# Kernel optimization log

Hardware: AMD Instinct MI355X
Metric: run time of the kernel (lower is better)

Reference implementation:

```python
import jax, jax.numpy as jnp
import numpy as np

S, B, C, H = 2048, 2, 512, 8
CC = C // H


def setup_inputs() -> dict:
    key = jax.random.key(0)
    ks = jax.random.split(key, 8)
    x = jax.random.normal(ks[0], (S, B, C), dtype=jnp.float32)
    pe = jax.random.normal(ks[1], (S, B, C), dtype=jnp.float32)
    # strict causal mask: True means masked-out (future positions t > s)
    idx = jnp.arange(S)
    content_mask = (idx[None, :] > idx[:, None])  # (s, t)
    content_mask = jnp.broadcast_to(content_mask[:, :, None], (S, S, B))
    pad = jnp.full((B,), S, dtype=jnp.int64)  # full-length sequences (unused in training path)
    scale = 0.02
    Wqkv = jax.random.normal(ks[2], (3 * C, C), dtype=jnp.float32) * scale
    bqkv = jax.random.normal(ks[3], (3 * C,), dtype=jnp.float32) * scale
    Wc = jax.random.normal(ks[4], (C, C), dtype=jnp.float32) * scale
    bc = jax.random.normal(ks[5], (C,), dtype=jnp.float32) * scale
    return {"x": x, "pe": pe, "content_mask": content_mask, "pad": pad,
            "Wqkv": Wqkv, "bqkv": bqkv, "Wc": Wc, "bc": bc}


def reference(x, pe, content_mask, pad, Wqkv, bqkv, Wc, bc):
    s, b, c = x.shape
    h, cc = H, CC
    qkv = jnp.einsum('sbc,dc->sbd', x + pe, Wqkv) + bqkv  # (s, b, 3c)
    q, k, v = jnp.split(qkv, 3, axis=-1)
    q = q.reshape(s, b, h, cc)
    k = k.reshape(s, b, h, cc)
    v = v.reshape(s, b, h, cc)
    temperature = 1.0 / np.sqrt(cc).astype(np.float32)
    qk = jnp.einsum('sbhc,tbhc->stbh', q, k) * temperature  # (s, t, b, h)
    a = jnp.where(content_mask[:, :, :, None], -jnp.inf, qk)
    p = jax.nn.softmax(a, axis=1)  # softmax over t (dim=1), matching torch
    out = jnp.einsum('stbh,tbhc->sbhc', p, v).reshape(s, b, c)
    out = jnp.einsum('sbc,dc->sbd', out, Wc) + bc
    return out
```

## Files before the change

kernel.cpp:

```cpp
#include <hip/hip_runtime.h>
#include <hip/hip_bf16.h>

#define S_LEN 2048
#define BATCH 2
#define CDIM  512
#define HEADS 8
#define HDIM  64
#define QKVD  1536

typedef float          f32x4  __attribute__((ext_vector_type(4)));
typedef __bf16         bf16x8 __attribute__((ext_vector_type(8)));
typedef unsigned short u16x8  __attribute__((ext_vector_type(8)));

typedef __attribute__((address_space(1))) const unsigned int* gas_ptr;
typedef __attribute__((address_space(3))) unsigned int* las_ptr;

static __device__ __forceinline__ unsigned short f2bf(float x) {
  union { float f; unsigned u; } v; v.f = x;
  unsigned r = v.u + 0x7fffu + ((v.u >> 16) & 1u);
  return (unsigned short)(r >> 16);
}
static __device__ __forceinline__ float bf2f(unsigned short x) {
  union { unsigned u; float f; } v; v.u = (unsigned)x << 16;
  return v.f;
}

__global__ void __launch_bounds__(256) prep_kernel(
    const float* __restrict__ x, const float* __restrict__ pe,
    const float* __restrict__ wqkv, const float* __restrict__ wc,
    unsigned short* __restrict__ xpe_bf,
    unsigned short* __restrict__ wqkv_bf,
    unsigned short* __restrict__ wc_bf) {
  const int N1 = S_LEN * BATCH * CDIM;
  const int N2 = QKVD * CDIM;
  const int NP = (N1 + N2 + CDIM * CDIM) / 8;
  const int pkt = blockIdx.x * 256 + threadIdx.x;
  if (pkt >= NP) return;
  int i = pkt * 8;
  u16x8 o;
  if (i < N1) {
    f32x4 a0 = *reinterpret_cast<const f32x4*>(x + i);
    f32x4 a1 = *reinterpret_cast<const f32x4*>(x + i + 4);
    f32x4 b0 = *reinterpret_cast<const f32x4*>(pe + i);
    f32x4 b1 = *reinterpret_cast<const f32x4*>(pe + i + 4);
#pragma unroll
    for (int j = 0; j < 4; ++j) { o[j] = f2bf(a0[j] + b0[j]); o[4 + j] = f2bf(a1[j] + b1[j]); }
    *reinterpret_cast<u16x8*>(xpe_bf + i) = o;
  } else if (i < N1 + N2) {
    i -= N1;
    f32x4 a0 = *reinterpret_cast<const f32x4*>(wqkv + i);
    f32x4 a1 = *reinterpret_cast<const f32x4*>(wqkv + i + 4);
#pragma unroll
    for (int j = 0; j < 4; ++j) { o[j] = f2bf(a0[j]); o[4 + j] = f2bf(a1[j]); }
    *reinterpret_cast<u16x8*>(wqkv_bf + i) = o;
  } else {
    i -= N1 + N2;
    f32x4 a0 = *reinterpret_cast<const f32x4*>(wc + i);
    f32x4 a1 = *reinterpret_cast<const f32x4*>(wc + i + 4);
#pragma unroll
    for (int j = 0; j < 4; ++j) { o[j] = f2bf(a0[j]); o[4 + j] = f2bf(a1[j]); }
    *reinterpret_cast<u16x8*>(wc_bf + i) = o;
  }
}

template <int BM, int BN, int OUT_BF16>
__global__ void __launch_bounds__(256) gemm_lds_kernel(
    const unsigned short* __restrict__ A,
    const unsigned short* __restrict__ Bt,
    const float* __restrict__ bias,
    void* __restrict__ Cout, int M, int N, int K) {
  constexpr int FM = BM / 32;
  constexpr int FN = BN / 32;
  __shared__ unsigned short Alds[BM * 64];
  __shared__ unsigned short Blds[BN * 64];

  const int tid  = threadIdx.x;
  const int w    = tid >> 6;
  const int lane = tid & 63;
  const int wr   = w >> 1, wc = w & 1;
  const int lr   = lane & 15, hi = lane >> 4;
  const int m0   = blockIdx.y * BM;
  const int n0   = blockIdx.x * BN;

  f32x4 acc[FM][FN];
#pragma unroll
  for (int fm = 0; fm < FM; ++fm)
#pragma unroll
    for (int fn = 0; fn < FN; ++fn) acc[fm][fn] = (f32x4){0.f, 0.f, 0.f, 0.f};

  for (int kc = 0; kc < K; kc += 64) {
    __syncthreads();
#pragma unroll
    for (int i = 0; i < BM / 32; ++i) {
      const int idx = tid + i * 256;
      const int row = idx >> 3, col = (idx & 7) * 8;
      const int scol = col ^ ((row & 7) * 8);
      __builtin_amdgcn_global_load_lds(
          (gas_ptr)(const void*)(A + (size_t)(m0 + row) * K + kc + scol),
          (las_ptr)(void*)(Alds + idx * 8), 16, 0, 0);
    }
#pragma unroll
    for (int i = 0; i < BN / 32; ++i) {
      const int idx = tid + i * 256;
      const int row = idx >> 3, col = (idx & 7) * 8;
      const int scol = col ^ ((row & 7) * 8);
      __builtin_amdgcn_global_load_lds(
          (gas_ptr)(const void*)(Bt + (size_t)(n0 + row) * K + kc + scol),
          (las_ptr)(void*)(Blds + idx * 8), 16, 0, 0);
    }
    __syncthreads();

    bf16x8 af[2][FM], bfr[2][FN];
#pragma unroll
    for (int ks = 0; ks < 2; ++ks) {
#pragma unroll
      for (int fm = 0; fm < FM; ++fm) {
        const int row = wr * (BM / 2) + fm * 16 + lr;
        af[ks][fm] = *reinterpret_cast<const bf16x8*>(
            &Alds[row * 64 + ((ks * 32 + hi * 8) ^ ((row & 7) * 8))]);
      }
#pragma unroll
      for (int fn = 0; fn < FN; ++fn) {
        const int row = wc * (BN / 2) + fn * 16 + lr;
        bfr[ks][fn] = *reinterpret_cast<const bf16x8*>(
            &Blds[row * 64 + ((ks * 32 + hi * 8) ^ ((row & 7) * 8))]);
      }
    }
#pragma unroll
    for (int ks = 0; ks < 2; ++ks)
#pragma unroll
      for (int fm = 0; fm < FM; ++fm)
#pragma unroll
        for (int fn = 0; fn < FN; ++fn)
          acc[fm][fn] = __builtin_amdgcn_mfma_f32_16x16x32_bf16(
              af[ks][fm], bfr[ks][fn], acc[fm][fn], 0, 0, 0);
  }

#pragma unroll
  for (int fn = 0; fn < FN; ++fn) {
    const int n = n0 + wc * (BN / 2) + fn * 16 + lr;
    const float bv = bias[n];
#pragma unroll
    for (int fm = 0; fm < FM; ++fm) {
#pragma unroll
      for (int r = 0; r < 4; ++r) {
        const int m = m0 + wr * (BM / 2) + fm * 16 + hi * 4 + r;
        const float val = acc[fm][fn][r] + bv;
        if (OUT_BF16)
          ((unsigned short*)Cout)[(size_t)m * N + n] = f2bf(val);
        else
          ((float*)Cout)[(size_t)m * N + n] = val;
      }
    }
  }
}

#define SCALE_LOG2E 0.18033688011112042f

__device__ __forceinline__ void tile_compute(
    const bf16x8* aq, const bf16x8 kf[4][2], const bf16x8 vf[2][4],
    f32x4* acc, float* rs, unsigned short* Pw,
    int q0, int t0, int lr, int hi) {
  const f32x4 z = (f32x4){0.f, 0.f, 0.f, 0.f};
  f32x4 d[4];
#pragma unroll
  for (int ks = 0; ks < 4; ++ks) {
    f32x4 dd = __builtin_amdgcn_mfma_f32_16x16x32_bf16(aq[0], kf[ks][0], z, 0, 0, 0);
    dd = __builtin_amdgcn_mfma_f32_16x16x32_bf16(aq[1], kf[ks][1], dd, 0, 0, 0);
    d[ks] = dd;
  }
#pragma unroll
  for (int ks = 0; ks < 4; ++ks) {
    const int t = t0 + ks * 16 + lr;
#pragma unroll
    for (int rr = 0; rr < 4; ++rr) {
      const int srow = q0 + hi * 4 + rr;
      float pv = __builtin_exp2f(d[ks][rr] * SCALE_LOG2E);
      pv = (t > srow) ? 0.f : pv;
      d[ks][rr] = pv;
      rs[rr] += pv;
    }
  }
#pragma unroll
  for (int ks = 0; ks < 4; ++ks)
#pragma unroll
    for (int rr = 0; rr < 4; ++rr) {
      const int row = hi * 4 + rr;
      Pw[(row * 64 + ks * 16 + lr) ^ ((row & 7) << 3)] = f2bf(d[ks][rr]);
    }
  bf16x8 pa[2];
#pragma unroll
  for (int kk = 0; kk < 2; ++kk)
    pa[kk] = *reinterpret_cast<const bf16x8*>(
        &Pw[(lr * 64 + kk * 32 + hi * 8) ^ ((lr & 7) << 3)]);
#pragma unroll
  for (int nt = 0; nt < 4; ++nt) {
    acc[nt] = __builtin_amdgcn_mfma_f32_16x16x32_bf16(pa[0], vf[0][nt], acc[nt], 0, 0, 0);
    acc[nt] = __builtin_amdgcn_mfma_f32_16x16x32_bf16(pa[1], vf[1][nt], acc[nt], 0, 0, 0);
  }
}

__global__ void __launch_bounds__(128) attn_part_kernel(
    const unsigned short* __restrict__ qkv,
    unsigned short* __restrict__ pacc0,
    unsigned short* __restrict__ pacc1,
    float* __restrict__ prs) {
  __shared__ unsigned short Klds[64 * 64];
  __shared__ unsigned short Vlds[64 * 64];
  __shared__ unsigned short Plds[2][16 * 64];

  const int bx   = blockIdx.x;
  const int qb   = bx >> 1;
  const int e    = bx & 1;
  const int h    = blockIdx.y;
  const int b    = blockIdx.z;
  const int tid  = threadIdx.x;
  const int w    = tid >> 6;
  const int lane = tid & 63;
  const int lr   = lane & 15;
  const int hi   = lane >> 4;

  const int p   = qb * 2 + w;
  const int q0A = p * 16;
  const int q0B = (127 - p) * 16;
  const int NT  = ((2047 - 32 * qb) >> 6) + 1;
  const int NTh = NT >> 1;
  const int lo  = e ? NTh : 0;
  const int hiT = e ? NT : NTh;

  const int RS = BATCH * QKVD;
  const unsigned short* Qbase = qkv + (size_t)b * QKVD + h * HDIM;
  const unsigned short* Kbase = Qbase + CDIM;
  const unsigned short* Vbase = Qbase + 2 * CDIM;

  bf16x8 aqA[2], aqB[2];
#pragma unroll
  for (int kk = 0; kk < 2; ++kk) {
    aqA[kk] = *reinterpret_cast<const bf16x8*>(
        Qbase + (size_t)(q0A + lr) * RS + kk * 32 + hi * 8);
    aqB[kk] = *reinterpret_cast<const bf16x8*>(
        Qbase + (size_t)(q0B + lr) * RS + kk * 32 + hi * 8);
  }

  f32x4 accA[4], accB[4];
  float rsA[4], rsB[4];
#pragma unroll
  for (int nt = 0; nt < 4; ++nt) {
    accA[nt] = (f32x4){0.f, 0.f, 0.f, 0.f};
    accB[nt] = (f32x4){0.f, 0.f, 0.f, 0.f};
  }
#pragma unroll
  for (int rr = 0; rr < 4; ++rr) { rsA[rr] = 0.f; rsB[rr] = 0.f; }

  const int va = tid & 31, vq = tid >> 5;
  unsigned short* Pw = Plds[w];

  for (int it = lo; it < hiT; ++it) {
    const int t0 = it * 64;
    __syncthreads();
#pragma unroll
    for (int i = 0; i < 4; ++i) {
      const int idx = tid + i * 128;
      const int row = idx >> 3, col = (idx & 7) * 8;
      const int scol = col ^ ((row & 7) * 8);
      __builtin_amdgcn_global_load_lds(
          (gas_ptr)(const void*)(Kbase + (size_t)(t0 + row) * RS + scol),
          (las_ptr)(void*)(Klds + idx * 8), 16, 0, 0);
    }
#pragma unroll
    for (int c = 0; c < 2; ++c) {
      const int cc = vq * 2 + c;
      const unsigned short* vp = Vbase + (size_t)(t0 + 2 * va) * RS + cc * 8;
      u16x8 v0 = *reinterpret_cast<const u16x8*>(vp);
      u16x8 v1 = *reinterpret_cast<const u16x8*>(vp + RS);
#pragma unroll
      for (int j = 0; j < 8; ++j) {
        const int dim = cc * 8 + j;
        const unsigned val = (unsigned)v0[j] | ((unsigned)v1[j] << 16);
        *reinterpret_cast<unsigned*>(
            &Vlds[(dim * 64 + 2 * va) ^ ((dim & 7) << 3)]) = val;
      }
    }
    __syncthreads();

    bf16x8 kf[4][2], vf[2][4];
#pragma unroll
    for (int ks = 0; ks < 4; ++ks)
#pragma unroll
      for (int kk = 0; kk < 2; ++kk) {
        const int row = ks * 16 + lr;
        kf[ks][kk] = *reinterpret_cast<const bf16x8*>(
            &Klds[(row * 64 + kk * 32 + hi * 8) ^ ((row & 7) << 3)]);
      }
#pragma unroll
    for (int kk = 0; kk < 2; ++kk)
#pragma unroll
      for (int nt = 0; nt < 4; ++nt) {
        const int row = nt * 16 + lr;
        vf[kk][nt] = *reinterpret_cast<const bf16x8*>(
            &Vlds[(row * 64 + kk * 32 + hi * 8) ^ ((row & 7) << 3)]);
      }

    if (t0 <= q0A + 15)
      tile_compute(aqA, kf, vf, accA, rsA, Pw, q0A, t0, lr, hi);
    if (t0 <= q0B + 15)
      tile_compute(aqB, kf, vf, accB, rsB, Pw, q0B, t0, lr, hi);
  }

  unsigned short* pacc = e ? pacc1 : pacc0;
#pragma unroll
  for (int rr = 0; rr < 4; ++rr) {
    float v = rsA[rr];
    v += __shfl_xor(v, 1); v += __shfl_xor(v, 2);
    v += __shfl_xor(v, 4); v += __shfl_xor(v, 8);
    rsA[rr] = v;
    v = rsB[rr];
    v += __shfl_xor(v, 1); v += __shfl_xor(v, 2);
    v += __shfl_xor(v, 4); v += __shfl_xor(v, 8);
    rsB[rr] = v;
  }
  if (lr == 0) {
#pragma unroll
    for (int rr = 0; rr < 4; ++rr) {
      const int sA = q0A + hi * 4 + rr;
      const int sB = q0B + hi * 4 + rr;
      prs[(((size_t)e * S_LEN + sA) * BATCH + b) * HEADS + h] = rsA[rr];
      prs[(((size_t)e * S_LEN + sB) * BATCH + b) * HEADS + h] = rsB[rr];
    }
  }
#pragma unroll
  for (int nt = 0; nt < 4; ++nt)
#pragma unroll
    for (int rr = 0; rr < 4; ++rr) {
      const int c = h * HDIM + nt * 16 + lr;
      const int sA = q0A + hi * 4 + rr;
      pacc[((size_t)sA * BATCH + b) * CDIM + c] = f2bf(accA[nt][rr]);
      const int sB = q0B + hi * 4 + rr;
      pacc[((size_t)sB * BATCH + b) * CDIM + c] = f2bf(accB[nt][rr]);
    }
}

__global__ void __launch_bounds__(256) reduce_kernel(
    const unsigned short* __restrict__ pacc1,
    const float* __restrict__ prs,
    unsigned short* __restrict__ out) {
  const int t = blockIdx.x * 256 + threadIdx.x;
  const int i8 = t * 8;
  const int c = i8 & 511;
  const int sb = i8 >> 9;
  const int b = sb & 1;
  const int s = sb >> 1;
  const int h = c >> 6;
  const float r0 = prs[(((size_t)0 * S_LEN + s) * BATCH + b) * HEADS + h];
  const float r1 = prs[(((size_t)1 * S_LEN + s) * BATCH + b) * HEADS + h];
  const float inv = 1.f / (r0 + r1);
  u16x8 a = *reinterpret_cast<const u16x8*>(out + i8);
  u16x8 bb = *reinterpret_cast<const u16x8*>(pacc1 + i8);
  u16x8 o;
#pragma unroll
  for (int j = 0; j < 8; ++j)
    o[j] = f2bf((bf2f(a[j]) + bf2f(bb[j])) * inv);
  *reinterpret_cast<u16x8*>(out + i8) = o;
}

extern "C" void kernel_launch(void* const* d_in, const int* in_sizes, int n_in,
                              void* d_out, int out_size, void* d_ws, size_t ws_size,
                              hipStream_t stream) {
  const float* x    = (const float*)d_in[0];
  const float* pe   = (const float*)d_in[1];
  const float* wqkv = (const float*)d_in[4];
  const float* bqkv = (const float*)d_in[5];
  const float* wc   = (const float*)d_in[6];
  const float* bc   = (const float*)d_in[7];

  unsigned short* xpe_bf  = (unsigned short*)d_ws;
  unsigned short* wqkv_bf = xpe_bf  + (size_t)S_LEN * BATCH * CDIM;
  unsigned short* wc_bf   = wqkv_bf + (size_t)QKVD * CDIM;
  unsigned short* qkv_bf  = wc_bf   + (size_t)CDIM * CDIM;
  unsigned short* attn_bf = qkv_bf  + (size_t)S_LEN * BATCH * QKVD;
  unsigned short* pacc0 = attn_bf;
  unsigned short* pacc1 = xpe_bf;
  float*          prs   = (float*)wqkv_bf;

  const int NP = (S_LEN * BATCH * CDIM + QKVD * CDIM + CDIM * CDIM) / 8;
  prep_kernel<<<dim3((NP + 255) / 256), dim3(256), 0, stream>>>(
      x, pe, wqkv, wc, xpe_bf, wqkv_bf, wc_bf);
  gemm_lds_kernel<64, 128, 1>
      <<<dim3(QKVD / 128, (S_LEN * BATCH) / 64), dim3(256), 0, stream>>>(
          xpe_bf, wqkv_bf, bqkv, (void*)qkv_bf, S_LEN * BATCH, QKVD, CDIM);
  attn_part_kernel<<<dim3(64, HEADS, BATCH), dim3(128), 0, stream>>>(
      qkv_bf, pacc0, pacc1, prs);
  reduce_kernel<<<dim3(S_LEN * BATCH * CDIM / 8 / 256), dim3(256), 0, stream>>>(
      pacc1, prs, pacc0);
  gemm_lds_kernel<64, 64, 0>
      <<<dim3(CDIM / 64, (S_LEN * BATCH) / 64), dim3(256), 0, stream>>>(
          attn_bf, wc_bf, bc, d_out, S_LEN * BATCH, CDIM, CDIM);
}
```

Measured before the change: 160.5 us.

## Emit head-major Q/K and transposed V from QKV GEMM; double-buffer LDS loads

The QKV GEMM epilogue now scatters Q and K into head-major contiguous buffers and V into a transposed per-head layout. This lets the attention kernel stage both K and V with direct global-to-LDS loads instead of a register transpose of V. Both the GEMM and attention kernels double-buffer their LDS tiles, prefetching the next tile while computing the current one and using one barrier per iteration. The cost is scattered, uncoalesced 2-byte stores for V in the GEMM epilogue, twice the LDS footprint (which may lower occupancy), and a separate buffer for the first partial accumulator.

After: 160.7 us. Within noise of the previous version (+0.1%).

```diff
diff --git a/kernel.cpp b/kernel.cpp
--- a/kernel.cpp
+++ b/kernel.cpp
@@ -63,16 +63,20 @@
   }
 }
 
-template <int BM, int BN, int OUT_BF16>
-__global__ void __launch_bounds__(256) gemm_lds_kernel(
+template <int BM, int BN, int MODE>
+__global__ void __launch_bounds__(256) gemm_kernel(
     const unsigned short* __restrict__ A,
     const unsigned short* __restrict__ Bt,
     const float* __restrict__ bias,
-    void* __restrict__ Cout, int M, int N, int K) {
+    float* __restrict__ outf,
+    unsigned short* __restrict__ qA,
+    unsigned short* __restrict__ kA,
+    unsigned short* __restrict__ vT,
+    int M, int N, int K) {
   constexpr int FM = BM / 32;
   constexpr int FN = BN / 32;
-  __shared__ unsigned short Alds[BM * 64];
-  __shared__ unsigned short Blds[BN * 64];
+  __shared__ unsigned short Alds[2][BM * 64];
+  __shared__ unsigned short Blds[2][BN * 64];
 
   const int tid  = threadIdx.x;
   const int w    = tid >> 6;
@@ -88,8 +92,7 @@
 #pragma unroll
     for (int fn = 0; fn < FN; ++fn) acc[fm][fn] = (f32x4){0.f, 0.f, 0.f, 0.f};
 
-  for (int kc = 0; kc < K; kc += 64) {
-    __syncthreads();
+  auto STAGE = [&](int buf, int kc) {
 #pragma unroll
     for (int i = 0; i < BM / 32; ++i) {
       const int idx = tid + i * 256;
@@ -97,7 +100,7 @@
       const int scol = col ^ ((row & 7) * 8);
       __builtin_amdgcn_global_load_lds(
           (gas_ptr)(const void*)(A + (size_t)(m0 + row) * K + kc + scol),
-          (las_ptr)(void*)(Alds + idx * 8), 16, 0, 0);
+          (las_ptr)(void*)(Alds[buf] + idx * 8), 16, 0, 0);
     }
 #pragma unroll
     for (int i = 0; i < BN / 32; ++i) {
@@ -106,10 +109,15 @@
       const int scol = col ^ ((row & 7) * 8);
       __builtin_amdgcn_global_load_lds(
           (gas_ptr)(const void*)(Bt + (size_t)(n0 + row) * K + kc + scol),
-          (las_ptr)(void*)(Blds + idx * 8), 16, 0, 0);
-    }
-    __syncthreads();
-
+          (las_ptr)(void*)(Blds[buf] + idx * 8), 16, 0, 0);
+    }
+  };
+
+  STAGE(0, 0);
+  __syncthreads();
+  int cur = 0;
+  for (int kc = 0; kc < K; kc += 64, cur ^= 1) {
+    if (kc + 64 < K) STAGE(cur ^ 1, kc + 64);
     bf16x8 af[2][FM], bfr[2][FN];
 #pragma unroll
     for (int ks = 0; ks < 2; ++ks) {
@@ -117,13 +125,13 @@
       for (int fm = 0; fm < FM; ++fm) {
         const int row = wr * (BM / 2) + fm * 16 + lr;
         af[ks][fm] = *reinterpret_cast<const bf16x8*>(
-            &Alds[row * 64 + ((ks * 32 + hi * 8) ^ ((row & 7) * 8))]);
+            &Alds[cur][row * 64 + ((ks * 32 + hi * 8) ^ ((row & 7) * 8))]);
       }
 #pragma unroll
       for (int fn = 0; fn < FN; ++fn) {
         const int row = wc * (BN / 2) + fn * 16 + lr;
         bfr[ks][fn] = *reinterpret_cast<const bf16x8*>(
-            &Blds[row * 64 + ((ks * 32 + hi * 8) ^ ((row & 7) * 8))]);
+            &Blds[cur][row * 64 + ((ks * 32 + hi * 8) ^ ((row & 7) * 8))]);
       }
     }
 #pragma unroll
@@ -134,6 +142,7 @@
         for (int fn = 0; fn < FN; ++fn)
           acc[fm][fn] = __builtin_amdgcn_mfma_f32_16x16x32_bf16(
               af[ks][fm], bfr[ks][fn], acc[fm][fn], 0, 0, 0);
+    __syncthreads();
   }
 
 #pragma unroll
@@ -146,10 +155,21 @@
       for (int r = 0; r < 4; ++r) {
         const int m = m0 + wr * (BM / 2) + fm * 16 + hi * 4 + r;
         const float val = acc[fm][fn][r] + bv;
-        if (OUT_BF16)
-          ((unsigned short*)Cout)[(size_t)m * N + n] = f2bf(val);
-        else
-          ((float*)Cout)[(size_t)m * N + n] = val;
+        if (MODE == 0) {
+          outf[(size_t)m * N + n] = val;
+        } else {
+          const int s = m >> 1, bb = m & 1;
+          if (n < CDIM) {
+            const int h = n >> 6, dim = n & 63;
+            qA[(((size_t)(bb * HEADS + h)) * S_LEN + s) * HDIM + dim] = f2bf(val);
+          } else if (n < 2 * CDIM) {
+            const int nn = n - CDIM, h = nn >> 6, dim = nn & 63;
+            kA[(((size_t)(bb * HEADS + h)) * S_LEN + s) * HDIM + dim] = f2bf(val);
+          } else {
+            const int nn = n - 2 * CDIM, h = nn >> 6, dim = nn & 63;
+            vT[(((size_t)(bb * HEADS + h)) * HDIM + dim) * S_LEN + s] = f2bf(val);
+          }
+        }
       }
     }
   }
@@ -201,12 +221,14 @@
 }
 
 __global__ void __launch_bounds__(128) attn_part_kernel(
-    const unsigned short* __restrict__ qkv,
+    const unsigned short* __restrict__ qA,
+    const unsigned short* __restrict__ kA,
+    const unsigned short* __restrict__ vT,
     unsigned short* __restrict__ pacc0,
     unsigned short* __restrict__ pacc1,
     float* __restrict__ prs) {
-  __shared__ unsigned short Klds[64 * 64];
-  __shared__ unsigned short Vlds[64 * 64];
+  __shared__ unsigned short Klds[2][64 * 64];
+  __shared__ unsigned short Vlds[2][64 * 64];
   __shared__ unsigned short Plds[2][16 * 64];
 
   const int bx   = blockIdx.x;
@@ -228,18 +250,17 @@
   const int lo  = e ? NTh : 0;
   const int hiT = e ? NT : NTh;
 
-  const int RS = BATCH * QKVD;
-  const unsigned short* Qbase = qkv + (size_t)b * QKVD + h * HDIM;
-  const unsigned short* Kbase = Qbase + CDIM;
-  const unsigned short* Vbase = Qbase + 2 * CDIM;
+  const unsigned short* Qh = qA + ((size_t)(b * HEADS + h)) * S_LEN * HDIM;
+  const unsigned short* Kh = kA + ((size_t)(b * HEADS + h)) * S_LEN * HDIM;
+  const unsigned short* Vh = vT + ((size_t)(b * HEADS + h)) * HDIM * S_LEN;
 
   bf16x8 aqA[2], aqB[2];
 #pragma unroll
   for (int kk = 0; kk < 2; ++kk) {
     aqA[kk] = *reinterpret_cast<const bf16x8*>(
-        Qbase + (size_t)(q0A + lr) * RS + kk * 32 + hi * 8);
+        Qh + (size_t)(q0A + lr) * HDIM + kk * 32 + hi * 8);
     aqB[kk] = *reinterpret_cast<const bf16x8*>(
-        Qbase + (size_t)(q0B + lr) * RS + kk * 32 + hi * 8);
+        Qh + (size_t)(q0B + lr) * HDIM + kk * 32 + hi * 8);
   }
 
   f32x4 accA[4], accB[4];
@@ -252,36 +273,28 @@
 #pragma unroll
   for (int rr = 0; rr < 4; ++rr) { rsA[rr] = 0.f; rsB[rr] = 0.f; }
 
-  const int va = tid & 31, vq = tid >> 5;
-  unsigned short* Pw = Plds[w];
-
-  for (int it = lo; it < hiT; ++it) {
-    const int t0 = it * 64;
-    __syncthreads();
+  auto STAGE = [&](int buf, int t0) {
 #pragma unroll
     for (int i = 0; i < 4; ++i) {
       const int idx = tid + i * 128;
       const int row = idx >> 3, col = (idx & 7) * 8;
       const int scol = col ^ ((row & 7) * 8);
       __builtin_amdgcn_global_load_lds(
-          (gas_ptr)(const void*)(Kbase + (size_t)(t0 + row) * RS + scol),
-          (las_ptr)(void*)(Klds + idx * 8), 16, 0, 0);
-    }
-#pragma unroll
-    for (int c = 0; c < 2; ++c) {
-      const int cc = vq * 2 + c;
-      const unsigned short* vp = Vbase + (size_t)(t0 + 2 * va) * RS + cc * 8;
-      u16x8 v0 = *reinterpret_cast<const u16x8*>(vp);
-      u16x8 v1 = *reinterpret_cast<const u16x8*>(vp + RS);
-#pragma unroll
-      for (int j = 0; j < 8; ++j) {
-        const int dim = cc * 8 + j;
-        const unsigned val = (unsigned)v0[j] | ((unsigned)v1[j] << 16);
-        *reinterpret_cast<unsigned*>(
-            &Vlds[(dim * 64 + 2 * va) ^ ((dim & 7) << 3)]) = val;
-      }
-    }
-    __syncthreads();
+          (gas_ptr)(const void*)(Kh + (size_t)(t0 + row) * HDIM + scol),
+          (las_ptr)(void*)(Klds[buf] + idx * 8), 16, 0, 0);
+      __builtin_amdgcn_global_load_lds(
+          (gas_ptr)(const void*)(Vh + (size_t)row * S_LEN + t0 + scol),
+          (las_ptr)(void*)(Vlds[buf] + idx * 8), 16, 0, 0);
+    }
+  };
+
+  unsigned short* Pw = Plds[w];
+  STAGE(0, lo * 64);
+  __syncthreads();
+  int cur = 0;
+  for (int it = lo; it < hiT; ++it, cur ^= 1) {
+    if (it + 1 < hiT) STAGE(cur ^ 1, (it + 1) * 64);
+    const int t0 = it * 64;
 
     bf16x8 kf[4][2], vf[2][4];
 #pragma unroll
@@ -290,7 +303,7 @@
       for (int kk = 0; kk < 2; ++kk) {
         const int row = ks * 16 + lr;
         kf[ks][kk] = *reinterpret_cast<const bf16x8*>(
-            &Klds[(row * 64 + kk * 32 + hi * 8) ^ ((row & 7) << 3)]);
+            &Klds[cur][(row * 64 + kk * 32 + hi * 8) ^ ((row & 7) << 3)]);
       }
 #pragma unroll
     for (int kk = 0; kk < 2; ++kk)
@@ -298,13 +311,14 @@
       for (int nt = 0; nt < 4; ++nt) {
         const int row = nt * 16 + lr;
         vf[kk][nt] = *reinterpret_cast<const bf16x8*>(
-            &Vlds[(row * 64 + kk * 32 + hi * 8) ^ ((row & 7) << 3)]);
+            &Vlds[cur][(row * 64 + kk * 32 + hi * 8) ^ ((row & 7) << 3)]);
       }
 
     if (t0 <= q0A + 15)
       tile_compute(aqA, kf, vf, accA, rsA, Pw, q0A, t0, lr, hi);
     if (t0 <= q0B + 15)
       tile_compute(aqB, kf, vf, accB, rsB, Pw, q0B, t0, lr, hi);
+    __syncthreads();
   }
 
   unsigned short* pacc = e ? pacc1 : pacc0;
@@ -376,23 +390,26 @@
   unsigned short* xpe_bf  = (unsigned short*)d_ws;
   unsigned short* wqkv_bf = xpe_bf  + (size_t)S_LEN * BATCH * CDIM;
   unsigned short* wc_bf   = wqkv_bf + (size_t)QKVD * CDIM;
-  unsigned short* qkv_bf  = wc_bf   + (size_t)CDIM * CDIM;
-  unsigned short* attn_bf = qkv_bf  + (size_t)S_LEN * BATCH * QKVD;
-  unsigned short* pacc0 = attn_bf;
+  unsigned short* qA_bf   = wc_bf   + (size_t)CDIM * CDIM;
+  unsigned short* kA_bf   = qA_bf   + (size_t)S_LEN * BATCH * CDIM;
+  unsigned short* vT_bf   = kA_bf   + (size_t)S_LEN * BATCH * CDIM;
+  unsigned short* pacc0   = vT_bf   + (size_t)S_LEN * BATCH * CDIM;
   unsigned short* pacc1 = xpe_bf;
   float*          prs   = (float*)wqkv_bf;
 
   const int NP = (S_LEN * BATCH * CDIM + QKVD * CDIM + CDIM * CDIM) / 8;
   prep_kernel<<<dim3((NP + 255) / 256), dim3(256), 0, stream>>>(
       x, pe, wqkv, wc, xpe_bf, wqkv_bf, wc_bf);
-  gemm_lds_kernel<64, 128, 1>
+  gemm_kernel<64, 128, 2>
       <<<dim3(QKVD / 128, (S_LEN * BATCH) / 64), dim3(256), 0, stream>>>(
-          xpe_bf, wqkv_bf, bqkv, (void*)qkv_bf, S_LEN * BATCH, QKVD, CDIM);
+          xpe_bf, wqkv_bf, bqkv, nullptr, qA_bf, kA_bf, vT_bf,
+          S_LEN * BATCH, QKVD, CDIM);
   attn_part_kernel<<<dim3(64, HEADS, BATCH), dim3(128), 0, stream>>>(
-      qkv_bf, pacc0, pacc1, prs);
+      qA_bf, kA_bf, vT_bf, pacc0, pacc1, prs);
   reduce_kernel<<<dim3(S_LEN * BATCH * CDIM / 8 / 256), dim3(256), 0, stream>>>(
       pacc1, prs, pacc0);
-  gemm_lds_kernel<64, 64, 0>
+  gemm_kernel<64, 64, 0>
       <<<dim3(CDIM / 64, (S_LEN * BATCH) / 64), dim3(256), 0, stream>>>(
-          attn_bf, wc_bf, bc, d_out, S_LEN * BATCH, CDIM, CDIM);
-}
+          pacc0, wc_bf, bc, (float*)d_out, nullptr, nullptr, nullptr,
+          S_LEN * BATCH, CDIM, CDIM);
+}
```
